# Kernel optimization log

Measured on AMD Instinct MI355X. Metric: run time of the kernel, lower is better.

Reference implementation:

```python
import jax, jax.numpy as jnp
import numpy as np

B, S, D = 2, 2048, 1024
H, HD = 16, 64
FF = 4096
LOCAL_W, RAND_P = 256, 0.2
EPS = 1e-5
NEG = -9e15


def _linear_params(key, din, dout):
    kw, kb = jax.random.split(key)
    bound = 1.0 / np.sqrt(din)
    W = jax.random.uniform(kw, (din, dout), jnp.float32, -bound, bound)
    b = jax.random.uniform(kb, (dout,), jnp.float32, -bound, bound)
    return W, b


def setup_inputs() -> dict:
    key = jax.random.key(0)
    ks = jax.random.split(key, 10)
    x = jax.random.normal(ks[0], (B, S, D), jnp.float32)
    # local + random mask, as in create_local_mask
    i = np.arange(S)[:, None]
    j = np.arange(S)[None, :]
    local = (np.abs(i - j) <= LOCAL_W // 2)
    rnd = np.asarray(jax.random.bernoulli(ks[1], RAND_P, (S, S)))
    mask = jnp.asarray(np.logical_or(local, rnd).astype(np.int32))
    Wq, bq = _linear_params(ks[2], D, D)
    Wk, bk = _linear_params(ks[3], D, D)
    Wv, bv = _linear_params(ks[4], D, D)
    Wo, bo = _linear_params(ks[5], D, D)
    W1, b1 = _linear_params(ks[6], D, FF)
    W2, b2 = _linear_params(ks[7], FF, D)
    g1 = jnp.ones((D,), jnp.float32); be1 = jnp.zeros((D,), jnp.float32)
    g2 = jnp.ones((D,), jnp.float32); be2 = jnp.zeros((D,), jnp.float32)
    return dict(x=x, mask=mask, Wq=Wq, bq=bq, Wk=Wk, bk=bk, Wv=Wv, bv=bv,
                Wo=Wo, bo=bo, W1=W1, b1=b1, W2=W2, b2=b2,
                g1=g1, be1=be1, g2=g2, be2=be2)


def _layernorm(x, g, b):
    mu = jnp.mean(x, axis=-1, keepdims=True)
    var = jnp.mean(jnp.square(x - mu), axis=-1, keepdims=True)
    return (x - mu) * jax.lax.rsqrt(var + EPS) * g + b


def reference(x, mask, Wq, bq, Wk, bk, Wv, bv, Wo, bo, W1, b1, W2, b2, g1, be1, g2, be2):
    scale = jnp.float32(np.sqrt(HD))  # sqrt(head_dim), requires_grad=False
    q = x @ Wq + bq
    k = x @ Wk + bk
    v = x @ Wv + bv
    # faithful to original: view(B, heads, S, head_dim) WITHOUT transpose
    q = q.reshape(B, H, S, HD)
    k = k.reshape(B, H, S, HD)
    v = v.reshape(B, H, S, HD)
    scores = jnp.einsum('bhsd,bhtd->bhst', q / scale, k)  # [B,H,S,S]
    scores = jnp.where(mask == 0, jnp.float32(NEG), scores)
    probs = jax.nn.softmax(scores, axis=-1)
    av = jnp.einsum('bhst,bhtd->bhsd', probs, v)
    # faithful reshape back: view(B, S, head_dim*heads)
    attn_out = av.reshape(B, S, H * HD) @ Wo + bo
    x = _layernorm(x + attn_out, g1, be1)
    ffn = jax.nn.gelu(x @ W1 + b1, approximate=False) @ W2 + b2
    x = _layernorm(x + ffn, g2, be2)
    return x
```

## Files before the change

kernel.cpp:

```cpp
#include <hip/hip_runtime.h>
#include <cstdint>
#include <cstddef>

namespace {

constexpr int kS  = 2048;
constexpr int kD  = 1024;
constexpr int kHD = 64;
constexpr int kTOK = 4096;

typedef float f32x4 __attribute__((ext_vector_type(4)));
typedef __bf16 bf16x8 __attribute__((ext_vector_type(8)));
typedef unsigned short u16x8 __attribute__((ext_vector_type(8)));

__device__ __forceinline__ unsigned short f2b(float f){
  unsigned int u = __builtin_bit_cast(unsigned int, f);
  u += 0x7fffu + ((u >> 16) & 1u);
  return (unsigned short)(u >> 16);
}

__device__ __forceinline__ float b2f(unsigned short u){
  return __builtin_bit_cast(float, (unsigned)u << 16);
}

__device__ __forceinline__ bf16x8 ldfrag(const unsigned short* p){
  return __builtin_bit_cast(bf16x8, *(const u16x8*)p);
}

__device__ __forceinline__ float fexp2(float x){
#if __has_builtin(__builtin_amdgcn_exp2f)
  return __builtin_amdgcn_exp2f(x);
#else
  return exp2f(x);
#endif
}

__device__ __forceinline__ float fast_erf(float x){
  const float ax = fabsf(x);
#if __has_builtin(__builtin_amdgcn_rcpf)
  const float t = __builtin_amdgcn_rcpf(1.0f + 0.3275911f * ax);
#else
  const float t = 1.0f / (1.0f + 0.3275911f * ax);
#endif
  const float y = t * (0.254829592f + t * (-0.284496736f + t * (1.421413741f +
                  t * (-1.453152027f + t * 1.061405429f))));
  const float e = fexp2(-ax * ax * 1.4426950408889634f);
  return copysignf(1.0f - y * e, x);
}

__device__ __forceinline__ void gl_lds16(const void* g, void* l){
  __builtin_amdgcn_global_load_lds(
      (__attribute__((address_space(1))) void*)(void*)g,
      (__attribute__((address_space(3))) void*)l, 16, 0, 0);
}

__device__ __forceinline__ bf16x8 ld_swz(const unsigned short* tile, int row, int slot){
  return ldfrag(tile + row * 64 + (((slot ^ row) & 7) << 3));
}

__device__ __forceinline__ void stageK8(const unsigned short* Kg, unsigned short* lds,
                                        int tid, int t0){
  const int r = tid >> 3, sl = tid & 7;
  const int sabs = t0 + r;
  gl_lds16(Kg + (size_t)(sabs >> 4) * 3072 + (sabs & 15) * 64 + (((sl ^ r) & 7) << 3),
           (char*)lds + tid * 16);
}

__device__ __forceinline__ void stageV8(const unsigned short* Vh, unsigned short* lds,
                                        int tid, int t0){
  const int r = tid >> 3, sl = tid & 7;
  gl_lds16(Vh + (size_t)r * kS + t0 + (((sl ^ r) & 7) << 3),
           (char*)lds + tid * 16);
}

__global__ __launch_bounds__(256) void prep_misc_kern(const float* __restrict__ x,
                                                      unsigned short* __restrict__ xb,
                                                      const int* __restrict__ mask,
                                                      unsigned long long* __restrict__ mb,
                                                      const float* __restrict__ bq,
                                                      const float* __restrict__ bk,
                                                      const float* __restrict__ bv,
                                                      float* __restrict__ bqkv){
  const int b = blockIdx.x;
  if (b < 4096){
    const int i = b * 256 + threadIdx.x;
    float4 v = ((const float4*)x)[i];
    ((ushort4*)xb)[i] = make_ushort4(f2b(v.x), f2b(v.y), f2b(v.z), f2b(v.w));
  } else if (b < 20480){
    const int gw   = ((b - 4096) * 256 + threadIdx.x) >> 6;
    const int lane = threadIdx.x & 63;
    const int row  = gw >> 5, word = gw & 31;
    const int key  = ((lane >> 2) & 3) * 16 + ((lane >> 4) & 3) * 4 + (lane & 3);
    const int m = mask[(size_t)row * kS + word * 64 + key];
    const unsigned long long bl = __ballot(m != 0);
    if (lane == 0) mb[(size_t)row * 32 + word] = bl;
  } else {
    const int i = (b - 20480) * 256 + threadIdx.x;
    float v = (i < 1024) ? bq[i] : ((i < 2048) ? bk[i - 1024] : bv[i - 2048]);
    bqkv[i] = v;
  }
}

__global__ __launch_bounds__(256) void wtrans_all_kern(const float* __restrict__ Wq,
                                                       const float* __restrict__ Wk,
                                                       const float* __restrict__ Wv,
                                                       const float* __restrict__ Wo,
                                                       const float* __restrict__ W1,
                                                       const float* __restrict__ W2,
                                                       unsigned short* __restrict__ WqkvT,
                                                       unsigned short* __restrict__ WoT,
                                                       unsigned short* __restrict__ W1T,
                                                       unsigned short* __restrict__ W2T){
  const int b = blockIdx.x;
  const float* W; unsigned short* Wt; int K, N, nx, lb;
  if      (b < 1024){ W = Wq; Wt = WqkvT;                 K = 1024; N = 1024; nx = 32;  lb = b; }
  else if (b < 2048){ W = Wk; Wt = WqkvT + 1024 * 1024;   K = 1024; N = 1024; nx = 32;  lb = b - 1024; }
  else if (b < 3072){ W = Wv; Wt = WqkvT + 2048 * 1024;   K = 1024; N = 1024; nx = 32;  lb = b - 2048; }
  else if (b < 4096){ W = Wo; Wt = WoT;                   K = 1024; N = 1024; nx = 32;  lb = b - 3072; }
  else if (b < 8192){ W = W1; Wt = W1T;                   K = 1024; N = 4096; nx = 128; lb = b - 4096; }
  else              { W = W2; Wt = W2T;                   K = 4096; N = 1024; nx = 32;  lb = b - 8192; }
  __shared__ float t[32][33];
  const int n0 = (lb % nx) * 32, k0 = (lb / nx) * 32;
  const int tx = threadIdx.x & 31, ty = threadIdx.x >> 5;
  #pragma unroll
  for (int i = 0; i < 32; i += 8)
    t[ty + i][tx] = W[(size_t)(k0 + ty + i) * N + n0 + tx];
  __syncthreads();
  #pragma unroll
  for (int i = 0; i < 32; i += 8)
    Wt[(size_t)(n0 + ty + i) * K + k0 + tx] = f2b(t[tx][ty + i]);
}

__global__ __launch_bounds__(256) void vtrans_kern(const unsigned short* __restrict__ QKV,
                                                   unsigned short* __restrict__ Vt){
  __shared__ unsigned short t[64][65];
  int bh = blockIdx.y, s0 = blockIdx.x * 64;
  const int rowbase = (bh >> 4) * 2048 + (bh & 15) * 128;
  const unsigned short* Vg = QKV + (size_t)rowbase * 3072 + 2048;
  unsigned short* Vth = Vt + (size_t)bh * kHD * kS;
  int tx = threadIdx.x & 63, ty = threadIdx.x >> 6;
  #pragma unroll
  for (int i = 0; i < 64; i += 4){
    const int s = s0 + ty + i;
    t[ty + i][tx] = Vg[(size_t)(s >> 4) * 3072 + (s & 15) * 64 + tx];
  }
  __syncthreads();
  #pragma unroll
  for (int i = 0; i < 64; i += 4)
    Vth[(size_t)(ty + i) * kS + s0 + tx] = t[tx][ty + i];
}

template <int ACT_GELU, int SPLITK, int SCLQ>
__global__ __launch_bounds__(512, 2) void gemm256_kern(const unsigned short* __restrict__ A,
                                                       const unsigned short* __restrict__ Bt,
                                                       const float* __restrict__ bias,
                                                       unsigned short* __restrict__ C,
                                                       int M, int N, int K){
  __shared__ unsigned short As[2][2][128 * 64];
  __shared__ unsigned short Bs[2][2][128 * 64];
  int bid = blockIdx.y * gridDim.x + blockIdx.x;
  const int nwg = gridDim.x * gridDim.y;
  bid = (bid & 7) * (nwg >> 3) + (bid >> 3);
  const int bx = bid % gridDim.x, by = bid / gridDim.x;
  const int m0 = by << 8, n0 = bx << 8;
  const int tid  = threadIdx.x;
  const int wave = tid >> 6, lane = tid & 63;
  const int wr = wave >> 2, wc = wave & 3;
  const int lr = lane & 15, lk = lane >> 4;
  const int kz   = K / SPLITK;
  const int kbeg = (SPLITK > 1) ? blockIdx.z * kz : 0;
  const int NT   = kz >> 6;
  const int srow = tid >> 3;
  const int scol = ((tid & 7) ^ (srow & 7)) << 3;
  const unsigned short* Ag = A  + (size_t)(m0 + srow) * K + kbeg + scol;
  const unsigned short* Bg = Bt + (size_t)(n0 + srow) * K + kbeg + scol;
  const int dst = tid * 8;
  const int sk0 = ((    lk) ^ (lr & 7)) << 3;
  const int sk1 = ((4 + lk) ^ (lr & 7)) << 3;
  const int aro = lr * 64;
  const int bro = ((wc & 1) * 64 + lr) * 64;
  const int bh_ = wc >> 1;

  f32x4 acc[8][4] = {};
  bf16x8 aR[4][2], bR[2][2][2];

  auto stA = [&](int b, int h, int kt){
    const unsigned short* s = Ag + (size_t)(h * 128) * K + kt * 64;
    gl_lds16(s,                  &As[b][h][dst]);
    gl_lds16(s + (size_t)64 * K, &As[b][h][4096 + dst]);
  };
  auto stB = [&](int b, int h, int kt){
    const unsigned short* s = Bg + (size_t)(h * 128) * K + kt * 64;
    gl_lds16(s,                  &Bs[b][h][dst]);
    gl_lds16(s + (size_t)64 * K, &Bs[b][h][4096 + dst]);
  };

#define LOAD_A(b, MH) { \
  _Pragma("unroll") for (int mp = 0; mp < 4; ++mp){ \
    aR[mp][0] = ldfrag(&As[b][wr][aro + ((MH) * 64 + mp * 16) * 64 + sk0]); \
    aR[mp][1] = ldfrag(&As[b][wr][aro + ((MH) * 64 + mp * 16) * 64 + sk1]); } }
#define LOAD_B(b, NH) { \
  _Pragma("unroll") for (int np = 0; np < 2; ++np){ \
    bR[NH][np][0] = ldfrag(&Bs[b][bh_][bro + ((NH) * 32 + np * 16) * 64 + sk0]); \
    bR[NH][np][1] = ldfrag(&Bs[b][bh_][bro + ((NH) * 32 + np * 16) * 64 + sk1]); } }
#define QMFMA(MH, NH) { \
  _Pragma("unroll") for (int kk = 0; kk < 2; ++kk) \
  _Pragma("unroll") for (int mp = 0; mp < 4; ++mp) \
  _Pragma("unroll") for (int np = 0; np < 2; ++np) \
    acc[(MH)*4+mp][(NH)*2+np] = __builtin_amdgcn_mfma_f32_16x16x32_bf16( \
        aR[mp][kk], bR[NH][np][kk], acc[(MH)*4+mp][(NH)*2+np], 0, 0, 0); }
#define PHASE_TAIL(QM) \
  asm volatile("s_barrier" ::: "memory"); \
  asm volatile("s_waitcnt lgkmcnt(0)" ::: "memory"); \
  __builtin_amdgcn_sched_barrier(0); \
  __builtin_amdgcn_s_setprio(1); \
  QM; \
  __builtin_amdgcn_s_setprio(0); \
  __builtin_amdgcn_sched_barrier(0); \
  asm volatile("s_barrier" ::: "memory");

  stA(0, 0, 0); stB(0, 0, 0); stB(0, 1, 0); stA(0, 1, 0);
  asm volatile("s_waitcnt vmcnt(4)" ::: "memory");
  asm volatile("s_barrier" ::: "memory");

  for (int t = 0; t < NT; ++t){
    const int b = t & 1, bn = b ^ 1;
    const bool pf = (t + 1 < NT);
    LOAD_A(b, 0); LOAD_B(b, 0);
    if (pf){ stA(bn, 0, t + 1); asm volatile("s_waitcnt vmcnt(4)" ::: "memory"); }
    else   {                    asm volatile("s_waitcnt vmcnt(2)" ::: "memory"); }
    PHASE_TAIL(QMFMA(0, 0));
    LOAD_B(b, 1);
    if (pf){ stB(bn, 0, t + 1); asm volatile("s_waitcnt vmcnt(4)" ::: "memory"); }
    else   {                    asm volatile("s_waitcnt vmcnt(0)" ::: "memory"); }
    PHASE_TAIL(QMFMA(0, 1));
    LOAD_A(b, 1);
    if (pf){ stB(bn, 1, t + 1); }
    PHASE_TAIL(QMFMA(1, 0));
    if (pf){ stA(bn, 1, t + 1); asm volatile("s_waitcnt vmcnt(4)" ::: "memory"); }
    PHASE_TAIL(QMFMA(1, 1));
  }
#undef LOAD_A
#undef LOAD_B
#undef QMFMA
#undef PHASE_TAIL

  unsigned short* Cb = C + (SPLITK > 1 ? (size_t)blockIdx.z * M * N : 0);
  float bvv[4], csc[4];
  #pragma unroll
  for (int n = 0; n < 4; ++n){
    const int col = n0 + wc * 64 + n * 16 + lr;
    bvv[n] = (SPLITK == 1) ? bias[col] : 0.0f;
    csc[n] = (SCLQ && col < 1024) ? 0.18033688011112042f : 1.0f;
  }
  #pragma unroll
  for (int m = 0; m < 8; ++m){
    #pragma unroll
    for (int j = 0; j < 4; ++j){
      const int row = m0 + wr * 128 + m * 16 + lk * 4 + j;
      unsigned short* crow = Cb + (size_t)row * N + n0 + wc * 64 + lr;
      #pragma unroll
      for (int n = 0; n < 4; ++n){
        float v = acc[m][n][j] + bvv[n];
        if (ACT_GELU) v = 0.5f * v * (1.0f + fast_erf(v * 0.70710678118654752f));
        if (SCLQ) v *= csc[n];
        crow[n * 16] = f2b(v);
      }
    }
  }
}

__global__ __launch_bounds__(512) void attn_kern(const unsigned short* __restrict__ QKV,
                                                 const unsigned short* __restrict__ Vt,
                                                 const unsigned long long* __restrict__ mbits,
                                                 unsigned short* __restrict__ O){
  __shared__ unsigned short Ks[2][64 * 64];
  __shared__ unsigned short Vs[2][64 * 64];
  __shared__ unsigned short Ps[8][16 * 64];
  const int tid = threadIdx.x;
  const int wave = tid >> 6, lane = tid & 63;
  const int lr = lane & 15, lk = lane >> 4;
  int bid = blockIdx.y * gridDim.x + blockIdx.x;
  bid = (bid & 7) * 64 + (bid >> 3);
  const int qblk = bid & 15, bh = bid >> 4;
  const int rowbase = (bh >> 4) * 2048 + (bh & 15) * 128;
  const unsigned short* Qg = QKV + (size_t)rowbase * 3072;
  const unsigned short* Kg = Qg + 1024;
  const unsigned short* Vh = Vt + (size_t)bh * kHD * kS;
  const int qbase = qblk * 128 + wave * 16;

  bf16x8 qf[2];
  { const int qr = qbase + lr;
    const unsigned short* qp = Qg + (size_t)(qr >> 4) * 3072 + (qr & 15) * 64 + lk * 8;
    qf[0] = ldfrag(qp); qf[1] = ldfrag(qp + 32); }

  f32x4 accO[4] = {};
  float lsum = 0.f;
  unsigned short* Pw = Ps[wave];
  char* Pwb = (char*)Pw + lr * 128 + ((lk & 1) << 3);
  const int lr7 = lr & 7;

  const unsigned long long* mrp = mbits + (size_t)(qbase + lr) * 32;
  unsigned long long mb = mrp[0];

  stageK8(Kg, Ks[0], tid, 0);
  stageV8(Vh, Vs[0], tid, 0);
  __syncthreads();

  int cur = 0;
  for (int t = 0; t < kS / 64; ++t){
    unsigned long long mbn = 0;
    if (t < kS / 64 - 1){
      stageK8(Kg, Ks[cur ^ 1], tid, (t + 1) * 64);
      stageV8(Vh, Vs[cur ^ 1], tid, (t + 1) * 64);
      mbn = mrp[t + 1];
    }
    f32x4 sa[4] = {};
    #pragma unroll
    for (int kk = 0; kk < 2; ++kk)
      #pragma unroll
      for (int n = 0; n < 4; ++n){
        bf16x8 kf = ld_swz(Ks[cur], n * 16 + lr, kk * 4 + lk);
        sa[n] = __builtin_amdgcn_mfma_f32_16x16x32_bf16(kf, qf[kk], sa[n], 0, 0, 0);
      }
    const unsigned wb = (unsigned)(mb >> (lk * 16));
    float s = 0.f;
    #pragma unroll
    for (int n = 0; n < 4; ++n){
      float p0, p1, p2, p3;
      {
        float v0 = fexp2(sa[n][0]), v1 = fexp2(sa[n][1]);
        float v2 = fexp2(sa[n][2]), v3 = fexp2(sa[n][3]);
        const int s0 = ((int)(wb << (31 - (n * 4 + 0)))) >> 31;
        const int s1 = ((int)(wb << (31 - (n * 4 + 1)))) >> 31;
        const int s2 = ((int)(wb << (31 - (n * 4 + 2)))) >> 31;
        const int s3 = ((int)(wb << (31 - (n * 4 + 3)))) >> 31;
        p0 = __builtin_bit_cast(float, __builtin_bit_cast(int, v0) & s0);
        p1 = __builtin_bit_cast(float, __builtin_bit_cast(int, v1) & s1);
        p2 = __builtin_bit_cast(float, __builtin_bit_cast(int, v2) & s2);
        p3 = __builtin_bit_cast(float, __builtin_bit_cast(int, v3) & s3);
      }
      s += (p0 + p1) + (p2 + p3);
      unsigned r0, r1;
      asm("v_cvt_pk_bf16_f32 %0, %1, %2" : "=v"(r0) : "v"(p0), "v"(p1));
      asm("v_cvt_pk_bf16_f32 %0, %1, %2" : "=v"(r1) : "v"(p2), "v"(p3));
      *(uint2*)(Pwb + (((2 * n + (lk >> 1)) ^ lr7) << 4)) = make_uint2(r0, r1);
    }
    s += __shfl_xor(s, 16);
    s += __shfl_xor(s, 32);
    lsum += s;
    #pragma unroll
    for (int kk = 0; kk < 2; ++kk){
      bf16x8 pf = ld_swz(Pw, lr, kk * 4 + lk);
      #pragma unroll
      for (int dd = 0; dd < 4; ++dd){
        bf16x8 vfr = ld_swz(Vs[cur], dd * 16 + lr, kk * 4 + lk);
        accO[dd] = __builtin_amdgcn_mfma_f32_16x16x32_bf16(pf, vfr, accO[dd], 0, 0, 0);
      }
    }
    mb = mbn;
    __syncthreads();
    cur ^= 1;
  }
  const size_t hoff = (size_t)bh * kS * kHD;
  #pragma unroll
  for (int j = 0; j < 4; ++j){
    const float inv = 1.0f / __shfl(lsum, lk * 4 + j);
    const int row = qbase + lk * 4 + j;
    #pragma unroll
    for (int dd = 0; dd < 4; ++dd)
      O[hoff + (size_t)row * 64 + dd * 16 + lr] = f2b(accO[dd][j] * inv);
  }
}

template <int NP, int PBF16, int OUT_B>
__global__ __launch_bounds__(256) void add_ln_kern(const float* __restrict__ X,
                                                   const void* __restrict__ P,
                                                   const float* __restrict__ bias,
                                                   const float* __restrict__ g,
                                                   const float* __restrict__ be,
                                                   float* __restrict__ Yf,
                                                   unsigned short* __restrict__ Yb){
  const int row = blockIdx.x;
  const int tid = threadIdx.x;
  const size_t pstride = (size_t)kTOK * kD;
  const int idx = row * 256 + tid;
  float r0 = 0.f, r1 = 0.f, r2 = 0.f, r3 = 0.f;
  #pragma unroll
  for (int z = 0; z < NP; ++z){
    if (PBF16){
      ushort4 u = ((const ushort4*)P)[z * (pstride / 4) + idx];
      r0 += b2f(u.x); r1 += b2f(u.y); r2 += b2f(u.z); r3 += b2f(u.w);
    } else {
      float4 p = ((const float4*)P)[z * (pstride / 4) + idx];
      r0 += p.x; r1 += p.y; r2 += p.z; r3 += p.w;
    }
  }
  const float4 bb = ((const float4*)bias)[tid];
  const float4 xv = ((const float4*)X)[idx];
  const float a0 = xv.x + r0 + bb.x, a1 = xv.y + r1 + bb.y;
  const float a2 = xv.z + r2 + bb.z, a3 = xv.w + r3 + bb.w;
  float s = a0 + a1 + a2 + a3;
  float q = a0*a0 + a1*a1 + a2*a2 + a3*a3;
  #pragma unroll
  for (int d = 1; d < 64; d <<= 1){ s += __shfl_xor(s, d); q += __shfl_xor(q, d); }
  __shared__ float red[8];
  const int wave = tid >> 6, lane = tid & 63;
  if (lane == 0){ red[wave] = s; red[4 + wave] = q; }
  __syncthreads();
  s = red[0] + red[1] + red[2] + red[3];
  q = red[4] + red[5] + red[6] + red[7];
  const float mu   = s * (1.0f / kD);
  const float var  = q * (1.0f / kD) - mu * mu;
  const float rstd = rsqrtf(var + 1e-5f);
  const float4 gv = ((const float4*)g)[tid];
  const float4 bv = ((const float4*)be)[tid];
  const float y0 = (a0 - mu) * rstd * gv.x + bv.x;
  const float y1 = (a1 - mu) * rstd * gv.y + bv.y;
  const float y2 = (a2 - mu) * rstd * gv.z + bv.z;
  const float y3 = (a3 - mu) * rstd * gv.w + bv.w;
  ((float4*)Yf)[idx] = make_float4(y0, y1, y2, y3);
  if (OUT_B)
    ((ushort4*)Yb)[idx] = make_ushort4(f2b(y0), f2b(y1), f2b(y2), f2b(y3));
}

}

extern "C" void kernel_launch(void* const* d_in, const int* in_sizes, int n_in,
                              void* d_out, int out_size, void* d_ws, size_t ws_size,
                              hipStream_t stream){
  (void)in_sizes; (void)n_in; (void)out_size;
  const float* x   = (const float*)d_in[0];
  const int*   mask= (const int*)d_in[1];
  const float* Wq  = (const float*)d_in[2];  const float* bq  = (const float*)d_in[3];
  const float* Wk  = (const float*)d_in[4];  const float* bk  = (const float*)d_in[5];
  const float* Wv  = (const float*)d_in[6];  const float* bv  = (const float*)d_in[7];
  const float* Wo  = (const float*)d_in[8];  const float* bo  = (const float*)d_in[9];
  const float* W1  = (const float*)d_in[10]; const float* b1  = (const float*)d_in[11];
  const float* W2  = (const float*)d_in[12]; const float* b2  = (const float*)d_in[13];
  const float* g1  = (const float*)d_in[14]; const float* be1 = (const float*)d_in[15];
  const float* g2  = (const float*)d_in[16]; const float* be2 = (const float*)d_in[17];

  char* ws = (char*)d_ws;
  const size_t MB = 1024 * 1024;
  if (ws_size < 96 * MB) return;

  unsigned short* W2T   = (unsigned short*)(ws + 0 * MB);
  unsigned short* W1T   = (unsigned short*)(ws + 8 * MB);
  unsigned short* WqkvT = (unsigned short*)(ws + 16 * MB);
  unsigned short* WoT   = (unsigned short*)(ws + 22 * MB);
  unsigned short* xb    = (unsigned short*)(ws + 24 * MB);
  unsigned short* qkv   = (unsigned short*)(ws + 32 * MB);
  unsigned short* vt    = (unsigned short*)(ws + 56 * MB);
  unsigned short* av    = (unsigned short*)(ws + 64 * MB);
  unsigned long long* mbits = (unsigned long long*)(ws + 72 * MB);
  float* bqkv           = (float*)(ws + 80 * MB);
  unsigned short* woP   = (unsigned short*)(ws + 32 * MB);
  float* y32            = (float*)(ws + 72 * MB);
  unsigned short* yb    = (unsigned short*)(ws + 88 * MB);
  unsigned short* hb    = (unsigned short*)(ws + 40 * MB);
  unsigned short* w2p   = (unsigned short*)(ws + 8 * MB);

  dim3 blk(256), gblk(512);
  wtrans_all_kern<<<dim3(12288), blk, 0, stream>>>(Wq, Wk, Wv, Wo, W1, W2,
                                                   WqkvT, WoT, W1T, W2T);
  prep_misc_kern<<<dim3(20492), blk, 0, stream>>>(x, xb, mask, mbits, bq, bk, bv, bqkv);

  gemm256_kern<0,1,1><<<dim3(12, 16), gblk, 0, stream>>>(xb, WqkvT, bqkv, qkv, 4096, 3072, 1024);

  vtrans_kern<<<dim3(32, 32), blk, 0, stream>>>(qkv, vt);
  attn_kern<<<dim3(16, 32), gblk, 0, stream>>>(qkv, vt, mbits, av);

  gemm256_kern<0,4,0><<<dim3(4, 16, 4), gblk, 0, stream>>>(av, WoT, bo, woP, 4096, 1024, 1024);
  add_ln_kern<4,1,1><<<dim3(4096), blk, 0, stream>>>(x, woP, bo, g1, be1, y32, yb);

  gemm256_kern<1,1,0><<<dim3(16, 16), gblk, 0, stream>>>(yb, W1T, b1, hb, 4096, 4096, 1024);
  gemm256_kern<0,4,0><<<dim3(4, 16, 4), gblk, 0, stream>>>(hb, W2T, b2, w2p, 4096, 1024, 4096);
  add_ln_kern<4,1,0><<<dim3(4096), blk, 0, stream>>>(y32, w2p, b2, g2, be2, (float*)d_out, nullptr);
}
```

Before: 241.5 us.

## Give each attention wave 32 query rows with half the waves per block

The attention kernel now runs 4 waves of 256 threads instead of 8 waves, and each wave handles two 16-row query tiles. Each K and V fragment read from LDS is reused for two MFMAs, which halves LDS fragment traffic per unit of compute. The K/V staging routines are rewritten so 256 threads still fill the 64x64 tiles, each thread issuing two loads. In exchange, registers per wave roughly double and there are fewer waves per block to hide latency.

```diff
diff --git a/kernel.cpp b/kernel.cpp
--- a/kernel.cpp
+++ b/kernel.cpp
@@ -58,19 +58,29 @@
   return ldfrag(tile + row * 64 + (((slot ^ row) & 7) << 3));
 }
 
-__device__ __forceinline__ void stageK8(const unsigned short* Kg, unsigned short* lds,
-                                        int tid, int t0){
-  const int r = tid >> 3, sl = tid & 7;
-  const int sabs = t0 + r;
-  gl_lds16(Kg + (size_t)(sabs >> 4) * 3072 + (sabs & 15) * 64 + (((sl ^ r) & 7) << 3),
-           (char*)lds + tid * 16);
-}
-
-__device__ __forceinline__ void stageV8(const unsigned short* Vh, unsigned short* lds,
-                                        int tid, int t0){
-  const int r = tid >> 3, sl = tid & 7;
-  gl_lds16(Vh + (size_t)r * kS + t0 + (((sl ^ r) & 7) << 3),
-           (char*)lds + tid * 16);
+__device__ __forceinline__ void stageKt(const unsigned short* Kg, unsigned short* lds,
+                                        int wave, int lane, int t0){
+  #pragma unroll
+  for (int i = 0; i < 2; ++i){
+    const int lin = i * 4096 + wave * 1024 + lane * 16;
+    const int r = lin >> 7;
+    const int sl = (lin >> 4) & 7;
+    const int sabs = t0 + r;
+    gl_lds16(Kg + (size_t)(sabs >> 4) * 3072 + (sabs & 15) * 64 + (((sl ^ r) & 7) << 3),
+             (char*)lds + i * 4096 + wave * 1024);
+  }
+}
+
+__device__ __forceinline__ void stageVt(const unsigned short* Vh, unsigned short* lds,
+                                        int wave, int lane, int t0){
+  #pragma unroll
+  for (int i = 0; i < 2; ++i){
+    const int lin = i * 4096 + wave * 1024 + lane * 16;
+    const int r = lin >> 7;
+    const int sl = (lin >> 4) & 7;
+    gl_lds16(Vh + (size_t)r * kS + t0 + (((sl ^ r) & 7) << 3),
+             (char*)lds + i * 4096 + wave * 1024);
+  }
 }
 
 __global__ __launch_bounds__(256) void prep_misc_kern(const float* __restrict__ x,
@@ -270,13 +280,13 @@
   }
 }
 
-__global__ __launch_bounds__(512) void attn_kern(const unsigned short* __restrict__ QKV,
+__global__ __launch_bounds__(256) void attn_kern(const unsigned short* __restrict__ QKV,
                                                  const unsigned short* __restrict__ Vt,
                                                  const unsigned long long* __restrict__ mbits,
                                                  unsigned short* __restrict__ O){
   __shared__ unsigned short Ks[2][64 * 64];
   __shared__ unsigned short Vs[2][64 * 64];
-  __shared__ unsigned short Ps[8][16 * 64];
+  __shared__ unsigned short Ps[4][32 * 64];
   const int tid = threadIdx.x;
   const int wave = tid >> 6, lane = tid & 63;
   const int lr = lane & 15, lk = lane >> 4;
@@ -287,89 +297,102 @@
   const unsigned short* Qg = QKV + (size_t)rowbase * 3072;
   const unsigned short* Kg = Qg + 1024;
   const unsigned short* Vh = Vt + (size_t)bh * kHD * kS;
-  const int qbase = qblk * 128 + wave * 16;
-
-  bf16x8 qf[2];
-  { const int qr = qbase + lr;
+  const int qbase = qblk * 128 + wave * 32;
+
+  bf16x8 qf[2][2];
+  #pragma unroll
+  for (int m = 0; m < 2; ++m){
+    const int qr = qbase + m * 16 + lr;
     const unsigned short* qp = Qg + (size_t)(qr >> 4) * 3072 + (qr & 15) * 64 + lk * 8;
-    qf[0] = ldfrag(qp); qf[1] = ldfrag(qp + 32); }
-
-  f32x4 accO[4] = {};
-  float lsum = 0.f;
+    qf[m][0] = ldfrag(qp); qf[m][1] = ldfrag(qp + 32);
+  }
+
+  f32x4 accO[2][4] = {};
+  float lsum[2] = { 0.f, 0.f };
   unsigned short* Pw = Ps[wave];
-  char* Pwb = (char*)Pw + lr * 128 + ((lk & 1) << 3);
   const int lr7 = lr & 7;
 
-  const unsigned long long* mrp = mbits + (size_t)(qbase + lr) * 32;
-  unsigned long long mb = mrp[0];
-
-  stageK8(Kg, Ks[0], tid, 0);
-  stageV8(Vh, Vs[0], tid, 0);
+  const unsigned long long* mrp0 = mbits + (size_t)(qbase + lr) * 32;
+  const unsigned long long* mrp1 = mbits + (size_t)(qbase + 16 + lr) * 32;
+  unsigned long long mb0 = mrp0[0], mb1 = mrp1[0];
+
+  stageKt(Kg, Ks[0], wave, lane, 0);
+  stageVt(Vh, Vs[0], wave, lane, 0);
   __syncthreads();
 
   int cur = 0;
   for (int t = 0; t < kS / 64; ++t){
-    unsigned long long mbn = 0;
+    unsigned long long mbn0 = 0, mbn1 = 0;
     if (t < kS / 64 - 1){
-      stageK8(Kg, Ks[cur ^ 1], tid, (t + 1) * 64);
-      stageV8(Vh, Vs[cur ^ 1], tid, (t + 1) * 64);
-      mbn = mrp[t + 1];
+      stageKt(Kg, Ks[cur ^ 1], wave, lane, (t + 1) * 64);
+      stageVt(Vh, Vs[cur ^ 1], wave, lane, (t + 1) * 64);
+      mbn0 = mrp0[t + 1]; mbn1 = mrp1[t + 1];
     }
-    f32x4 sa[4] = {};
+    f32x4 sa[2][4] = {};
     #pragma unroll
     for (int kk = 0; kk < 2; ++kk)
       #pragma unroll
       for (int n = 0; n < 4; ++n){
         bf16x8 kf = ld_swz(Ks[cur], n * 16 + lr, kk * 4 + lk);
-        sa[n] = __builtin_amdgcn_mfma_f32_16x16x32_bf16(kf, qf[kk], sa[n], 0, 0, 0);
+        sa[0][n] = __builtin_amdgcn_mfma_f32_16x16x32_bf16(kf, qf[0][kk], sa[0][n], 0, 0, 0);
+        sa[1][n] = __builtin_amdgcn_mfma_f32_16x16x32_bf16(kf, qf[1][kk], sa[1][n], 0, 0, 0);
       }
-    const unsigned wb = (unsigned)(mb >> (lk * 16));
-    float s = 0.f;
     #pragma unroll
-    for (int n = 0; n < 4; ++n){
-      float p0, p1, p2, p3;
-      {
-        float v0 = fexp2(sa[n][0]), v1 = fexp2(sa[n][1]);
-        float v2 = fexp2(sa[n][2]), v3 = fexp2(sa[n][3]);
-        const int s0 = ((int)(wb << (31 - (n * 4 + 0)))) >> 31;
-        const int s1 = ((int)(wb << (31 - (n * 4 + 1)))) >> 31;
-        const int s2 = ((int)(wb << (31 - (n * 4 + 2)))) >> 31;
-        const int s3 = ((int)(wb << (31 - (n * 4 + 3)))) >> 31;
-        p0 = __builtin_bit_cast(float, __builtin_bit_cast(int, v0) & s0);
-        p1 = __builtin_bit_cast(float, __builtin_bit_cast(int, v1) & s1);
-        p2 = __builtin_bit_cast(float, __builtin_bit_cast(int, v2) & s2);
-        p3 = __builtin_bit_cast(float, __builtin_bit_cast(int, v3) & s3);
+    for (int m = 0; m < 2; ++m){
+      const unsigned wb = (unsigned)((m ? mb1 : mb0) >> (lk * 16));
+      char* Pwb = (char*)Pw + (m * 16 + lr) * 128 + ((lk & 1) << 3);
+      float s = 0.f;
+      #pragma unroll
+      for (int n = 0; n < 4; ++n){
+        float p0, p1, p2, p3;
+        {
+          float v0 = fexp2(sa[m][n][0]), v1 = fexp2(sa[m][n][1]);
+          float v2 = fexp2(sa[m][n][2]), v3 = fexp2(sa[m][n][3]);
+          const int s0 = ((int)(wb << (31 - (n * 4 + 0)))) >> 31;
+          const int s1 = ((int)(wb << (31 - (n * 4 + 1)))) >> 31;
+          const int s2 = ((int)(wb << (31 - (n * 4 + 2)))) >> 31;
+          const int s3 = ((int)(wb << (31 - (n * 4 + 3)))) >> 31;
+          p0 = __builtin_bit_cast(float, __builtin_bit_cast(int, v0) & s0);
+          p1 = __builtin_bit_cast(float, __builtin_bit_cast(int, v1) & s1);
+          p2 = __builtin_bit_cast(float, __builtin_bit_cast(int, v2) & s2);
+          p3 = __builtin_bit_cast(float, __builtin_bit_cast(int, v3) & s3);
+        }
+        s += (p0 + p1) + (p2 + p3);
+        unsigned r0, r1;
+        asm("v_cvt_pk_bf16_f32 %0, %1, %2" : "=v"(r0) : "v"(p0), "v"(p1));
+        asm("v_cvt_pk_bf16_f32 %0, %1, %2" : "=v"(r1) : "v"(p2), "v"(p3));
+        *(uint2*)(Pwb + (((2 * n + (lk >> 1)) ^ lr7) << 4)) = make_uint2(r0, r1);
       }
-      s += (p0 + p1) + (p2 + p3);
-      unsigned r0, r1;
-      asm("v_cvt_pk_bf16_f32 %0, %1, %2" : "=v"(r0) : "v"(p0), "v"(p1));
-      asm("v_cvt_pk_bf16_f32 %0, %1, %2" : "=v"(r1) : "v"(p2), "v"(p3));
-      *(uint2*)(Pwb + (((2 * n + (lk >> 1)) ^ lr7) << 4)) = make_uint2(r0, r1);
+      s += __shfl_xor(s, 16);
+      s += __shfl_xor(s, 32);
+      lsum[m] += s;
     }
-    s += __shfl_xor(s, 16);
-    s += __shfl_xor(s, 32);
-    lsum += s;
     #pragma unroll
     for (int kk = 0; kk < 2; ++kk){
-      bf16x8 pf = ld_swz(Pw, lr, kk * 4 + lk);
+      bf16x8 pf0 = ld_swz(Pw, lr,      kk * 4 + lk);
+      bf16x8 pf1 = ld_swz(Pw, 16 + lr, kk * 4 + lk);
       #pragma unroll
       for (int dd = 0; dd < 4; ++dd){
         bf16x8 vfr = ld_swz(Vs[cur], dd * 16 + lr, kk * 4 + lk);
-        accO[dd] = __builtin_amdgcn_mfma_f32_16x16x32_bf16(pf, vfr, accO[dd], 0, 0, 0);
+        accO[0][dd] = __builtin_amdgcn_mfma_f32_16x16x32_bf16(pf0, vfr, accO[0][dd], 0, 0, 0);
+        accO[1][dd] = __builtin_amdgcn_mfma_f32_16x16x32_bf16(pf1, vfr, accO[1][dd], 0, 0, 0);
       }
     }
-    mb = mbn;
+    mb0 = mbn0; mb1 = mbn1;
     __syncthreads();
     cur ^= 1;
   }
   const size_t hoff = (size_t)bh * kS * kHD;
   #pragma unroll
-  for (int j = 0; j < 4; ++j){
-    const float inv = 1.0f / __shfl(lsum, lk * 4 + j);
-    const int row = qbase + lk * 4 + j;
+  for (int m = 0; m < 2; ++m){
     #pragma unroll
-    for (int dd = 0; dd < 4; ++dd)
-      O[hoff + (size_t)row * 64 + dd * 16 + lr] = f2b(accO[dd][j] * inv);
+    for (int j = 0; j < 4; ++j){
+      const float inv = 1.0f / __shfl(lsum[m], lk * 4 + j);
+      const int row = qbase + m * 16 + lk * 4 + j;
+      #pragma unroll
+      for (int dd = 0; dd < 4; ++dd)
+        O[hoff + (size_t)row * 64 + dd * 16 + lr] = f2b(accO[m][dd][j] * inv);
+    }
   }
 }
 
@@ -469,7 +492,7 @@
   gemm256_kern<0,1,1><<<dim3(12, 16), gblk, 0, stream>>>(xb, WqkvT, bqkv, qkv, 4096, 3072, 1024);
 
   vtrans_kern<<<dim3(32, 32), blk, 0, stream>>>(qkv, vt);
-  attn_kern<<<dim3(16, 32), gblk, 0, stream>>>(qkv, vt, mbits, av);
+  attn_kern<<<dim3(16, 32), blk, 0, stream>>>(qkv, vt, mbits, av);
 
   gemm256_kern<0,4,0><<<dim3(4, 16, 4), gblk, 0, stream>>>(av, WoT, bo, woP, 4096, 1024, 1024);
   add_ln_kern<4,1,1><<<dim3(4096), blk, 0, stream>>>(x, woP, bo, g1, be1, y32, yb);
```

After: 249.0 us. +3.1%, slower.
